# Kernel tuning notes

Hardware: AMD Instinct MI355X
Metric: run time of the kernel (lower is better)

Reference implementation:

```python
import jax, jax.numpy as jnp
import numpy as np

N_NODES = 50000
N_EDGES = 800000
D = 256


def setup_inputs() -> dict:
    key = jax.random.key(0)
    k_x, k_e, k_w1, k_w2 = jax.random.split(key, 4)
    x = jax.random.normal(k_x, (N_NODES, D), dtype=jnp.float32)
    edge_index = jax.random.randint(k_e, (2, N_EDGES), 0, N_NODES, dtype=jnp.int64)
    # attention MLP params (Linear(d, d//2) -> ReLU -> Linear(d//2, 1) -> Sigmoid)
    W1 = jax.random.normal(k_w1, (D, D // 2), dtype=jnp.float32) * (1.0 / np.sqrt(D))
    b1 = jnp.zeros((D // 2,), dtype=jnp.float32)
    W2 = jax.random.normal(k_w2, (D // 2, 1), dtype=jnp.float32) * (1.0 / np.sqrt(D // 2))
    b2 = jnp.zeros((1,), dtype=jnp.float32)
    return {"x": x, "edge_index": edge_index, "W1": W1, "b1": b1, "W2": W2, "b2": b2}


def reference(x, edge_index, W1, b1, W2, b2):
    # mean aggregation with attention: for each destination node i (row),
    # weighted mean of neighbor (col) features with sigmoid-MLP attention weights.
    row, col = edge_index[0], edge_index[1]
    neigh = x[col]                                   # [E, D] gathered neighbor features
    h = jax.nn.relu(neigh @ W1 + b1)                 # [E, D//2]
    w = jax.nn.sigmoid(h @ W2 + b2)                  # [E, 1] attention weight per edge
    num = jax.ops.segment_sum(neigh * w, row, num_segments=N_NODES)  # [N, D]
    den = jax.ops.segment_sum(w, row, num_segments=N_NODES)          # [N, 1]
    # nodes with no neighbors stay zero (matching the torch loop's skip)
    out = jnp.where(den > 0, num / jnp.maximum(den, 1e-12), 0.0)
    return out
```

## Files before the change

kernel.cpp:

```cpp
#include <hip/hip_runtime.h>
#include <hip/hip_bf16.h>

#define D 256
#define DH 128
#define NB 8

typedef __attribute__((ext_vector_type(8))) short short8;
typedef __attribute__((ext_vector_type(4))) float floatx4;
typedef __attribute__((ext_vector_type(4))) unsigned int uintx4;

__device__ __forceinline__ int eload(const void* p, long long i, int is64) {
    if (is64) return (int)((const long long*)p)[i];
    return ((const int*)p)[i];
}

__device__ __forceinline__ unsigned pack_bf16(unsigned a, unsigned b) {
    unsigned ra = (a + 0x7fffu + ((a >> 16) & 1u)) >> 16;
    unsigned rb = (b + 0x7fffu + ((b >> 16) & 1u)) & 0xffff0000u;
    return ra | rb;
}
__device__ __forceinline__ unsigned short bf16_of(float f) {
    unsigned u = __float_as_uint(f);
    return (unsigned short)((u + 0x7fffu + ((u >> 16) & 1u)) >> 16);
}

__global__ __launch_bounds__(256) void prep_kernel(const float* __restrict__ W1,
                                                   uint4* __restrict__ Bp,
                                                   const int* __restrict__ ei,
                                                   int* __restrict__ flag, int E,
                                                   int* __restrict__ cursor,
                                                   int N, int pad) {
    if (blockIdx.x >= 17) {
        int total4 = (N * pad) >> 2;
        uint4* c4 = (uint4*)cursor;
        uint4 z = make_uint4(0u, 0u, 0u, 0u);
        for (int i = (blockIdx.x - 17) * 256 + threadIdx.x; i < total4;
             i += (gridDim.x - 17) * 256)
            c4[i] = z;
        if (blockIdx.x == 17 && threadIdx.x == 0) {
            for (int i = total4 * 4; i < N * pad; ++i) cursor[i] = 0;
        }
        return;
    }
    if (blockIdx.x == 16) {
        int tid = threadIdx.x;
        if (tid == 0) *flag = 0;
        __syncthreads();
        int limit = min(E, 4096);
        int v = 0;
        for (int i = tid; i < limit; i += 256) v |= ei[2 * i + 1];
#pragma unroll
        for (int off = 32; off > 0; off >>= 1) v |= __shfl_down(v, off, 64);
        if ((tid & 63) == 0) atomicOr(flag, v);
        return;
    }
    int t = blockIdx.x * 256 + threadIdx.x;
    int lane = t & 63;
    int kt = (t >> 6) & 7;
    int nt = t >> 9;
    int col = nt * 16 + (lane & 15);
    int k0 = kt * 32 + (lane >> 4) * 8;
    unsigned v[8];
#pragma unroll
    for (int j = 0; j < 8; ++j) v[j] = __float_as_uint(W1[(k0 + j) * DH + col]);
    uint4 o;
    o.x = pack_bf16(v[0], v[1]);
    o.y = pack_bf16(v[2], v[3]);
    o.z = pack_bf16(v[4], v[5]);
    o.w = pack_bf16(v[6], v[7]);
    Bp[t] = o;
}

__global__ __launch_bounds__(256) void score_scatter_kernel(
        const float* __restrict__ x, const uint4* __restrict__ Bp,
        const float* __restrict__ b1, const float* __restrict__ W2,
        const float* __restrict__ b2, uint2* __restrict__ xb,
        float* __restrict__ s,
        const void* __restrict__ ep, const int* __restrict__ flag,
        int* __restrict__ cursor, unsigned short* __restrict__ cols,
        int cap, int pad, int N, int E, int SB) {
    if ((int)blockIdx.x >= SB) {
        int is64 = (*flag == 0);
        int base = (blockIdx.x - SB) * 2048 + threadIdx.x;
        int r[8], c[8];
        bool vld[8];
#pragma unroll
        for (int j = 0; j < 8; ++j) {
            int e = base + j * 256;
            vld[j] = (e < E);
            if (vld[j]) {
                r[j] = eload(ep, e, is64);
                c[j] = eload(ep, (long long)E + e, is64);
            }
        }
#pragma unroll
        for (int j = 0; j < 8; ++j) {
            if (vld[j]) {
                int p = atomicAdd(&cursor[r[j] * pad], 1);
                if (p < cap)
                    __builtin_nontemporal_store((unsigned short)c[j],
                                                &cols[(size_t)r[j] * cap + p]);
            }
        }
        return;
    }

    __shared__ __align__(16) uint2 lds[64 * 64];
    int tid = threadIdx.x;
    int blk = blockIdx.x;
    long long n64 = (long long)N * 64;

    long long gbase = (long long)blk * 4096 + tid;
#pragma unroll
    for (int i = 0; i < 16; ++i) {
        long long g = gbase + i * 256;
        int idx = i * 256 + tid;
        if (g < n64) {
            uint4 f = ((const uint4*)x)[g];
            uint2 o;
            o.x = pack_bf16(f.x, f.y);
            o.y = pack_bf16(f.z, f.w);
            xb[g] = o;
            int row = idx >> 6, cc = idx & 63;
            lds[row * 64 + (cc ^ ((row & 7) << 1))] = o;
        }
    }
    __syncthreads();

    int lane = tid & 63;
    int wid = tid >> 6;
    int quad = lane >> 4;
    int rbase = blk * 64 + wid * 16;
    int lrow = wid * 16 + (lane & 15);
    int fx = (lrow & 7) << 1;

    short8 afrag[8];
#pragma unroll
    for (int kt = 0; kt < 8; ++kt) {
        int e = kt * 8 + quad * 2;
        afrag[kt] = *(const short8*)&lds[lrow * 64 + (e ^ fx)];
    }

    const short8* Bs = (const short8*)Bp;
    float z0 = 0.f, z1 = 0.f, z2 = 0.f, z3 = 0.f;
#pragma unroll
    for (int nt = 0; nt < 8; ++nt) {
        floatx4 acc = {0.f, 0.f, 0.f, 0.f};
#pragma unroll
        for (int kt = 0; kt < 8; ++kt) {
            short8 b = Bs[(nt * 8 + kt) * 64 + lane];
            acc = __builtin_amdgcn_mfma_f32_16x16x32_bf16(afrag[kt], b, acc, 0, 0, 0);
        }
        int col = nt * 16 + (lane & 15);
        float b1c = b1[col], w2c = W2[col];
        z0 += fmaxf(acc[0] + b1c, 0.f) * w2c;
        z1 += fmaxf(acc[1] + b1c, 0.f) * w2c;
        z2 += fmaxf(acc[2] + b1c, 0.f) * w2c;
        z3 += fmaxf(acc[3] + b1c, 0.f) * w2c;
    }

#pragma unroll
    for (int off = 1; off < 16; off <<= 1) {
        z0 += __shfl_xor(z0, off, 64);
        z1 += __shfl_xor(z1, off, 64);
        z2 += __shfl_xor(z2, off, 64);
        z3 += __shfl_xor(z3, off, 64);
    }
    if ((lane & 15) == 0) {
        float b2v = b2[0];
        int r = rbase + quad * 4;
        float zz[4] = {z0, z1, z2, z3};
#pragma unroll
        for (int j = 0; j < 4; ++j)
            if (r + j < N) s[r + j] = 1.f / (1.f + __expf(-(zz[j] + b2v)));
    }
}

__device__ __forceinline__ float4 unpack_bf16x4(uint2 v) {
    float4 r;
    r.x = __uint_as_float(v.x << 16);
    r.y = __uint_as_float(v.x & 0xffff0000u);
    r.z = __uint_as_float(v.y << 16);
    r.w = __uint_as_float(v.y & 0xffff0000u);
    return r;
}

__global__ __launch_bounds__(256) void agg_u16_kernel(const uint2* __restrict__ xb,
                                                      const float* __restrict__ s,
                                                      const int* __restrict__ cursor,
                                                      const unsigned short* __restrict__ cols,
                                                      int cap, int pad,
                                                      float4* __restrict__ out4, int N) {
    int lane = threadIdx.x & 63;
    int node = blockIdx.x * 4 + (threadIdx.x >> 6);
    if (node >= N) return;
    int cnt = min(cursor[node * pad], cap);
    const unsigned short* mc = cols + (size_t)node * cap;

    float4 acc = make_float4(0.f, 0.f, 0.f, 0.f);
    float den = 0.f;
    int k = 0;
    for (; k + 8 <= cnt; k += 8) {
        uintx4 cc = __builtin_nontemporal_load((const uintx4*)(mc + k));
        int c0 = cc.x & 0xffff, c1 = cc.x >> 16;
        int c2 = cc.y & 0xffff, c3 = cc.y >> 16;
        int c4 = cc.z & 0xffff, c5 = cc.z >> 16;
        int c6 = cc.w & 0xffff, c7 = cc.w >> 16;
        float s0 = s[c0], s1 = s[c1], s2 = s[c2], s3 = s[c3];
        float s4 = s[c4], s5 = s[c5], s6 = s[c6], s7 = s[c7];
        uint2 v0 = xb[(size_t)c0 * 64 + lane];
        uint2 v1 = xb[(size_t)c1 * 64 + lane];
        uint2 v2 = xb[(size_t)c2 * 64 + lane];
        uint2 v3 = xb[(size_t)c3 * 64 + lane];
        uint2 v4 = xb[(size_t)c4 * 64 + lane];
        uint2 v5 = xb[(size_t)c5 * 64 + lane];
        uint2 v6 = xb[(size_t)c6 * 64 + lane];
        uint2 v7 = xb[(size_t)c7 * 64 + lane];
        float4 f0 = unpack_bf16x4(v0);
        float4 f1 = unpack_bf16x4(v1);
        float4 f2 = unpack_bf16x4(v2);
        float4 f3 = unpack_bf16x4(v3);
        float4 f4 = unpack_bf16x4(v4);
        float4 f5 = unpack_bf16x4(v5);
        float4 f6 = unpack_bf16x4(v6);
        float4 f7 = unpack_bf16x4(v7);
        acc.x = fmaf(f0.x, s0, fmaf(f1.x, s1, fmaf(f2.x, s2, fmaf(f3.x, s3, acc.x))));
        acc.y = fmaf(f0.y, s0, fmaf(f1.y, s1, fmaf(f2.y, s2, fmaf(f3.y, s3, acc.y))));
        acc.z = fmaf(f0.z, s0, fmaf(f1.z, s1, fmaf(f2.z, s2, fmaf(f3.z, s3, acc.z))));
        acc.w = fmaf(f0.w, s0, fmaf(f1.w, s1, fmaf(f2.w, s2, fmaf(f3.w, s3, acc.w))));
        acc.x = fmaf(f4.x, s4, fmaf(f5.x, s5, fmaf(f6.x, s6, fmaf(f7.x, s7, acc.x))));
        acc.y = fmaf(f4.y, s4, fmaf(f5.y, s5, fmaf(f6.y, s6, fmaf(f7.y, s7, acc.y))));
        acc.z = fmaf(f4.z, s4, fmaf(f5.z, s5, fmaf(f6.z, s6, fmaf(f7.z, s7, acc.z))));
        acc.w = fmaf(f4.w, s4, fmaf(f5.w, s5, fmaf(f6.w, s6, fmaf(f7.w, s7, acc.w))));
        den += ((s0 + s1) + (s2 + s3)) + ((s4 + s5) + (s6 + s7));
    }
    for (; k + 4 <= cnt; k += 4) {
        uint2 cc = *(const uint2*)(mc + k);
        int c0 = cc.x & 0xffff, c1 = cc.x >> 16;
        int c2 = cc.y & 0xffff, c3 = cc.y >> 16;
        float s0 = s[c0], s1 = s[c1], s2 = s[c2], s3 = s[c3];
        uint2 v0 = xb[(size_t)c0 * 64 + lane];
        uint2 v1 = xb[(size_t)c1 * 64 + lane];
        uint2 v2 = xb[(size_t)c2 * 64 + lane];
        uint2 v3 = xb[(size_t)c3 * 64 + lane];
        float4 f0 = unpack_bf16x4(v0);
        float4 f1 = unpack_bf16x4(v1);
        float4 f2 = unpack_bf16x4(v2);
        float4 f3 = unpack_bf16x4(v3);
        acc.x = fmaf(f0.x, s0, fmaf(f1.x, s1, fmaf(f2.x, s2, fmaf(f3.x, s3, acc.x))));
        acc.y = fmaf(f0.y, s0, fmaf(f1.y, s1, fmaf(f2.y, s2, fmaf(f3.y, s3, acc.y))));
        acc.z = fmaf(f0.z, s0, fmaf(f1.z, s1, fmaf(f2.z, s2, fmaf(f3.z, s3, acc.z))));
        acc.w = fmaf(f0.w, s0, fmaf(f1.w, s1, fmaf(f2.w, s2, fmaf(f3.w, s3, acc.w))));
        den += (s0 + s1) + (s2 + s3);
    }
    for (; k < cnt; ++k) {
        int c0 = mc[k];
        float s0 = s[c0];
        float4 f0 = unpack_bf16x4(xb[(size_t)c0 * 64 + lane]);
        acc.x = fmaf(f0.x, s0, acc.x);
        acc.y = fmaf(f0.y, s0, acc.y);
        acc.z = fmaf(f0.z, s0, acc.z);
        acc.w = fmaf(f0.w, s0, acc.w);
        den += s0;
    }
    floatx4 o = {0.f, 0.f, 0.f, 0.f};
    if (cnt > 0) {
        float inv = 1.f / den;
        o.x = acc.x * inv; o.y = acc.y * inv; o.z = acc.z * inv; o.w = acc.w * inv;
    }
    __builtin_nontemporal_store(o, (floatx4*)&out4[(size_t)node * 64 + lane]);
}

__global__ __launch_bounds__(256) void detect_kernel(const int* __restrict__ ei,
                                                     int* __restrict__ flag, int E) {
    int tid = threadIdx.x;
    int limit = min(E, 4096);
    int v = 0;
    for (int i = tid; i < limit; i += 256) v |= ei[2 * i + 1];
#pragma unroll
    for (int off = 32; off > 0; off >>= 1) v |= __shfl_down(v, off, 64);
    if ((tid & 63) == 0) atomicOr(flag, v);
}

__global__ __launch_bounds__(256) void score_kernel(const float* __restrict__ x,
                                                    const float* __restrict__ W1,
                                                    const float* __restrict__ b1,
                                                    const float* __restrict__ W2,
                                                    const float* __restrict__ b2,
                                                    float* __restrict__ s, int N) {
    __shared__ __align__(16) float xs[4][NB][D];
    int lane = threadIdx.x & 63;
    int wid  = threadIdx.x >> 6;
    int base = (blockIdx.x * 4 + wid) * NB;
#pragma unroll
    for (int m = 0; m < NB; ++m) {
        int n = base + m;
        float4 v = make_float4(0.f, 0.f, 0.f, 0.f);
        if (n < N) v = ((const float4*)x)[(size_t)n * 64 + lane];
        ((float4*)&xs[wid][m][0])[lane] = v;
    }
    __syncthreads();
    float h0[NB], h1[NB];
#pragma unroll
    for (int m = 0; m < NB; ++m) { h0[m] = 0.f; h1[m] = 0.f; }
#pragma unroll 4
    for (int k = 0; k < D; ++k) {
        float w1a = W1[k * DH + lane];
        float w1b = W1[k * DH + 64 + lane];
#pragma unroll
        for (int m = 0; m < NB; ++m) {
            float xv = xs[wid][m][k];
            h0[m] = fmaf(xv, w1a, h0[m]);
            h1[m] = fmaf(xv, w1b, h1[m]);
        }
    }
    float b1a = b1[lane], b1b = b1[lane + 64];
    float w2a = W2[lane], w2b = W2[lane + 64];
    float b2v = b2[0];
#pragma unroll
    for (int m = 0; m < NB; ++m) {
        float za = fmaxf(h0[m] + b1a, 0.f) * w2a + fmaxf(h1[m] + b1b, 0.f) * w2b;
#pragma unroll
        for (int off = 32; off > 0; off >>= 1) za += __shfl_down(za, off, 64);
        if (lane == 0) {
            int n = base + m;
            if (n < N) s[n] = 1.f / (1.f + __expf(-(za + b2v)));
        }
    }
}

__global__ __launch_bounds__(256) void hist_kernel(const void* __restrict__ ep,
                                                   const int* __restrict__ flag,
                                                   int* __restrict__ cnt, int E) {
    int is64 = (*flag == 0);
    int e = blockIdx.x * blockDim.x + threadIdx.x;
    if (e < E) atomicAdd(&cnt[eload(ep, e, is64)], 1);
}

__global__ __launch_bounds__(256) void bucket_kernel(const int* __restrict__ cnt,
                                                     int* __restrict__ beg,
                                                     int* __restrict__ cursor,
                                                     int* __restrict__ total, int N) {
    int i = blockIdx.x * blockDim.x + threadIdx.x;
    int lane = threadIdx.x & 63;
    int v = (i < N) ? cnt[i] : 0;
    int inc = v;
#pragma unroll
    for (int off = 1; off < 64; off <<= 1) {
        int t = __shfl_up(inc, off, 64);
        if (lane >= off) inc += t;
    }
    int base = 0;
    if (lane == 63) base = atomicAdd(total, inc);
    base = __shfl(base, 63, 64);
    if (i < N) {
        int b = base + inc - v;
        beg[i] = b;
        cursor[i] = b;
    }
}

__global__ __launch_bounds__(256) void scatter32_kernel(const void* __restrict__ ep,
                                                        const int* __restrict__ flag,
                                                        int* __restrict__ cursor,
                                                        int* __restrict__ cols, int E) {
    int is64 = (*flag == 0);
    int e = blockIdx.x * blockDim.x + threadIdx.x;
    if (e < E) {
        int r = eload(ep, e, is64);
        int c = eload(ep, (long long)E + e, is64);
        int p = atomicAdd(&cursor[r], 1);
        cols[p] = c;
    }
}

__global__ __launch_bounds__(256) void agg_f32_kernel(const float4* __restrict__ x4,
                                                      const float* __restrict__ s,
                                                      const int* __restrict__ begs,
                                                      const int* __restrict__ cnt,
                                                      const int* __restrict__ cols,
                                                      float4* __restrict__ out4, int N) {
    int lane = threadIdx.x & 63;
    int node = blockIdx.x * 4 + (threadIdx.x >> 6);
    if (node >= N) return;
    int beg = begs[node], end = beg + cnt[node];
    float4 acc = make_float4(0.f, 0.f, 0.f, 0.f);
    float den = 0.f;
    for (int k = beg; k < end; ++k) {
        int c = cols[k];
        float sc = s[c];
        float4 xv = x4[(size_t)c * 64 + lane];
        acc.x = fmaf(xv.x, sc, acc.x);
        acc.y = fmaf(xv.y, sc, acc.y);
        acc.z = fmaf(xv.z, sc, acc.z);
        acc.w = fmaf(xv.w, sc, acc.w);
        den += sc;
    }
    float4 o = make_float4(0.f, 0.f, 0.f, 0.f);
    if (end > beg) {
        float inv = 1.f / den;
        o.x = acc.x * inv; o.y = acc.y * inv; o.z = acc.z * inv; o.w = acc.w * inv;
    }
    out4[(size_t)node * 64 + lane] = o;
}

extern "C" void kernel_launch(void* const* d_in, const int* in_sizes, int n_in,
                              void* d_out, int out_size, void* d_ws, size_t ws_size,
                              hipStream_t stream) {
    const float* x  = (const float*)d_in[0];
    const void*  ei = d_in[1];
    const float* W1 = (const float*)d_in[2];
    const float* b1 = (const float*)d_in[3];
    const float* W2 = (const float*)d_in[4];
    const float* b2 = (const float*)d_in[5];
    int N = in_sizes[0] / D;
    int E = in_sizes[1] / 2;

    char* ws = (char*)d_ws;

    auto plan = [&](int cap, int pad, size_t& oCur, size_t& oS, size_t& oCols,
                    size_t& oBp, size_t& oXb) -> size_t {
        oCur  = 16;
        oS    = (oCur + (size_t)N * pad * 4 + 15) & ~15ull;
        oCols = (oS + (size_t)N * 4 + 255) & ~255ull;
        oBp   = (oCols + (size_t)N * cap * 2 + 255) & ~255ull;
        oXb   = (oBp + 65536 + 255) & ~255ull;
        return oXb + (size_t)N * D * 2;
    };

    int cap = 96, pad = 16;
    size_t oCur, oS, oCols, oBp, oXb;
    size_t need = plan(cap, pad, oCur, oS, oCols, oBp, oXb);
    if (need > ws_size) { pad = 4;  need = plan(cap, pad, oCur, oS, oCols, oBp, oXb); }
    if (need > ws_size) { pad = 1;  need = plan(cap, pad, oCur, oS, oCols, oBp, oXb); }
    if (need > ws_size) { cap = 64; need = plan(cap, pad, oCur, oS, oCols, oBp, oXb); }

    if (N <= 65536 && need <= ws_size) {
        int*            flag   = (int*)(ws);
        int*            cursor = (int*)(ws + oCur);
        float*          s      = (float*)(ws + oS);
        unsigned short* cols   = (unsigned short*)(ws + oCols);
        uint4*          Bpack  = (uint4*)(ws + oBp);
        uint2*          xb     = (uint2*)(ws + oXb);

        const int ZB = 256;
        prep_kernel<<<17 + ZB, 256, 0, stream>>>(W1, Bpack, (const int*)ei, flag, E,
                                                 cursor, N, pad);

        int SB = (N + 63) / 64;
        int TBe = (E + 2047) / 2048;
        score_scatter_kernel<<<SB + TBe, 256, 0, stream>>>(x, Bpack, b1, W2, b2,
                                                           xb, s, ei, flag, cursor,
                                                           cols, cap, pad, N, E, SB);
        agg_u16_kernel<<<(N + 3) / 4, 256, 0, stream>>>(xb, s, cursor, cols, cap, pad,
                                                        (float4*)d_out, N);
        return;
    }

    size_t o0 = 0;
    size_t o1 = 16;
    size_t o2 = (o1 + (size_t)N * 4 + 15) & ~15ull;
    size_t o3 = (o2 + (size_t)N * 4 + 15) & ~15ull;
    size_t o4 = (o3 + (size_t)N * 4 + 15) & ~15ull;
    size_t o5 = (o4 + (size_t)N * 4 + 15) & ~15ull;
    int*   flag   = (int*)(ws + o0);
    int*   total  = (int*)(ws + o0 + 4);
    int*   cnt    = (int*)(ws + o1);
    int*   beg    = (int*)(ws + o2);
    int*   cursor = (int*)(ws + o3);
    float* s      = (float*)(ws + o4);
    int*   cols   = (int*)(ws + o5);

    hipMemsetAsync(ws, 0, o1 + (size_t)N * 4, stream);
    detect_kernel<<<1, 256, 0, stream>>>((const int*)ei, flag, E);
    score_kernel<<<(N + 4 * NB - 1) / (4 * NB), 256, 0, stream>>>(x, W1, b1, W2, b2, s, N);
    hist_kernel<<<(E + 255) / 256, 256, 0, stream>>>(ei, flag, cnt, E);
    bucket_kernel<<<(N + 255) / 256, 256, 0, stream>>>(cnt, beg, cursor, total, N);
    scatter32_kernel<<<(E + 255) / 256, 256, 0, stream>>>(ei, flag, cursor, cols, E);
    agg_f32_kernel<<<(N + 3) / 4, 256, 0, stream>>>((const float4*)x, s, beg, cnt, cols,
                                                    (float4*)d_out, N);
}
```

Baseline: 205.6 us.

## Slice-major bf16 feature layout with sentinel-filled adjacency and sliced aggregation

Stores the bf16 copy of x in eight 32-feature slices, each node-major, and splits aggregation so every block handles one slice. Within a wave, the eight lanes of each octet cover one neighbor, so eight neighbors are processed in parallel and then reduced with shuffles. The adjacency buffer is pre-filled with a 0xffff sentinel, so aggregation no longer reads the per-node counter. The score kernel reads its MFMA A-fragments back from global xb instead of LDS, and the per-node capacity drops from 96 to 64. This aims to improve gather locality and latency hiding, at the cost of reading the column lists eight times, an extra fill pass, and a limit of 65535 nodes.

New measurement: 298.7 us. 45.3% more time.

```diff
diff --git a/kernel.cpp b/kernel.cpp
--- a/kernel.cpp
+++ b/kernel.cpp
@@ -19,9 +19,14 @@
     unsigned rb = (b + 0x7fffu + ((b >> 16) & 1u)) & 0xffff0000u;
     return ra | rb;
 }
-__device__ __forceinline__ unsigned short bf16_of(float f) {
-    unsigned u = __float_as_uint(f);
-    return (unsigned short)((u + 0x7fffu + ((u >> 16) & 1u)) >> 16);
+
+__device__ __forceinline__ float4 unpack_bf16x4(uint2 v) {
+    float4 r;
+    r.x = __uint_as_float(v.x << 16);
+    r.y = __uint_as_float(v.x & 0xffff0000u);
+    r.z = __uint_as_float(v.y << 16);
+    r.w = __uint_as_float(v.y & 0xffff0000u);
+    return r;
 }
 
 __global__ __launch_bounds__(256) void prep_kernel(const float* __restrict__ W1,
@@ -29,16 +34,22 @@
                                                    const int* __restrict__ ei,
                                                    int* __restrict__ flag, int E,
                                                    int* __restrict__ cursor,
-                                                   int N, int pad) {
+                                                   unsigned short* __restrict__ cols,
+                                                   int cap, int N, int pad) {
     if (blockIdx.x >= 17) {
+        int stride = (gridDim.x - 17) * 256;
+        int tid0 = (blockIdx.x - 17) * 256 + threadIdx.x;
         int total4 = (N * pad) >> 2;
         uint4* c4 = (uint4*)cursor;
         uint4 z = make_uint4(0u, 0u, 0u, 0u);
-        for (int i = (blockIdx.x - 17) * 256 + threadIdx.x; i < total4;
-             i += (gridDim.x - 17) * 256)
-            c4[i] = z;
+        for (int i = tid0; i < total4; i += stride) c4[i] = z;
+        int colQ = (N * cap) >> 3;
+        uint4* q4 = (uint4*)cols;
+        uint4 f = make_uint4(~0u, ~0u, ~0u, ~0u);
+        for (int i = tid0; i < colQ; i += stride) q4[i] = f;
         if (blockIdx.x == 17 && threadIdx.x == 0) {
             for (int i = total4 * 4; i < N * pad; ++i) cursor[i] = 0;
+            for (int i = colQ * 8; i < N * cap; ++i) cols[i] = 0xffffu;
         }
         return;
     }
@@ -78,7 +89,7 @@
         float* __restrict__ s,
         const void* __restrict__ ep, const int* __restrict__ flag,
         int* __restrict__ cursor, unsigned short* __restrict__ cols,
-        int cap, int pad, int N, int E, int SB) {
+        int cap, int pad, int Npad, int N, int E, int SB) {
     if ((int)blockIdx.x >= SB) {
         int is64 = (*flag == 0);
         int base = (blockIdx.x - SB) * 2048 + threadIdx.x;
@@ -105,10 +116,10 @@
         return;
     }
 
-    __shared__ __align__(16) uint2 lds[64 * 64];
     int tid = threadIdx.x;
     int blk = blockIdx.x;
     long long n64 = (long long)N * 64;
+    int npad8 = Npad * 8;
 
     long long gbase = (long long)blk * 4096 + tid;
 #pragma unroll
@@ -116,13 +127,13 @@
         long long g = gbase + i * 256;
         int idx = i * 256 + tid;
         if (g < n64) {
-            uint4 f = ((const uint4*)x)[g];
+            uint4 fv = ((const uint4*)x)[g];
             uint2 o;
-            o.x = pack_bf16(f.x, f.y);
-            o.y = pack_bf16(f.z, f.w);
-            xb[g] = o;
+            o.x = pack_bf16(fv.x, fv.y);
+            o.y = pack_bf16(fv.z, fv.w);
             int row = idx >> 6, cc = idx & 63;
-            lds[row * 64 + (cc ^ ((row & 7) << 1))] = o;
+            int nodeid = blk * 64 + row;
+            xb[(size_t)(cc >> 3) * npad8 + (size_t)nodeid * 8 + (cc & 7)] = o;
         }
     }
     __syncthreads();
@@ -131,15 +142,12 @@
     int wid = tid >> 6;
     int quad = lane >> 4;
     int rbase = blk * 64 + wid * 16;
-    int lrow = wid * 16 + (lane & 15);
-    int fx = (lrow & 7) << 1;
+    int lnode = rbase + (lane & 15);
 
     short8 afrag[8];
 #pragma unroll
-    for (int kt = 0; kt < 8; ++kt) {
-        int e = kt * 8 + quad * 2;
-        afrag[kt] = *(const short8*)&lds[lrow * 64 + (e ^ fx)];
-    }
+    for (int kt = 0; kt < 8; ++kt)
+        afrag[kt] = *(const short8*)&xb[(size_t)kt * npad8 + (size_t)lnode * 8 + quad * 2];
 
     const short8* Bs = (const short8*)Bp;
     float z0 = 0.f, z1 = 0.f, z2 = 0.f, z3 = 0.f;
@@ -176,99 +184,65 @@
     }
 }
 
-__device__ __forceinline__ float4 unpack_bf16x4(uint2 v) {
-    float4 r;
-    r.x = __uint_as_float(v.x << 16);
-    r.y = __uint_as_float(v.x & 0xffff0000u);
-    r.z = __uint_as_float(v.y << 16);
-    r.w = __uint_as_float(v.y & 0xffff0000u);
-    return r;
-}
-
-__global__ __launch_bounds__(256) void agg_u16_kernel(const uint2* __restrict__ xb,
-                                                      const float* __restrict__ s,
-                                                      const int* __restrict__ cursor,
-                                                      const unsigned short* __restrict__ cols,
-                                                      int cap, int pad,
-                                                      float4* __restrict__ out4, int N) {
+__global__ __launch_bounds__(256) void agg_slice_kernel(
+        const uint2* __restrict__ xb, const float* __restrict__ s,
+        const unsigned short* __restrict__ cols,
+        int cap, int Npad, float4* __restrict__ out4, int N) {
+    int slice = blockIdx.x & 7;
+    int group = blockIdx.x >> 3;
+    int wid = threadIdx.x >> 6;
     int lane = threadIdx.x & 63;
-    int node = blockIdx.x * 4 + (threadIdx.x >> 6);
+    int oct = lane >> 3;
+    int dl  = lane & 7;
+    int node = group * 4 + wid;
     if (node >= N) return;
-    int cnt = min(cursor[node * pad], cap);
-    const unsigned short* mc = cols + (size_t)node * cap;
+
+    const uint4* mc4 = (const uint4*)(cols + (size_t)node * cap);
+    const uint2* xbs = xb + (size_t)slice * Npad * 8;
 
     float4 acc = make_float4(0.f, 0.f, 0.f, 0.f);
     float den = 0.f;
-    int k = 0;
-    for (; k + 8 <= cnt; k += 8) {
-        uintx4 cc = __builtin_nontemporal_load((const uintx4*)(mc + k));
-        int c0 = cc.x & 0xffff, c1 = cc.x >> 16;
-        int c2 = cc.y & 0xffff, c3 = cc.y >> 16;
-        int c4 = cc.z & 0xffff, c5 = cc.z >> 16;
-        int c6 = cc.w & 0xffff, c7 = cc.w >> 16;
-        float s0 = s[c0], s1 = s[c1], s2 = s[c2], s3 = s[c3];
-        float s4 = s[c4], s5 = s[c5], s6 = s[c6], s7 = s[c7];
-        uint2 v0 = xb[(size_t)c0 * 64 + lane];
-        uint2 v1 = xb[(size_t)c1 * 64 + lane];
-        uint2 v2 = xb[(size_t)c2 * 64 + lane];
-        uint2 v3 = xb[(size_t)c3 * 64 + lane];
-        uint2 v4 = xb[(size_t)c4 * 64 + lane];
-        uint2 v5 = xb[(size_t)c5 * 64 + lane];
-        uint2 v6 = xb[(size_t)c6 * 64 + lane];
-        uint2 v7 = xb[(size_t)c7 * 64 + lane];
-        float4 f0 = unpack_bf16x4(v0);
-        float4 f1 = unpack_bf16x4(v1);
-        float4 f2 = unpack_bf16x4(v2);
-        float4 f3 = unpack_bf16x4(v3);
-        float4 f4 = unpack_bf16x4(v4);
-        float4 f5 = unpack_bf16x4(v5);
-        float4 f6 = unpack_bf16x4(v6);
-        float4 f7 = unpack_bf16x4(v7);
-        acc.x = fmaf(f0.x, s0, fmaf(f1.x, s1, fmaf(f2.x, s2, fmaf(f3.x, s3, acc.x))));
-        acc.y = fmaf(f0.y, s0, fmaf(f1.y, s1, fmaf(f2.y, s2, fmaf(f3.y, s3, acc.y))));
-        acc.z = fmaf(f0.z, s0, fmaf(f1.z, s1, fmaf(f2.z, s2, fmaf(f3.z, s3, acc.z))));
-        acc.w = fmaf(f0.w, s0, fmaf(f1.w, s1, fmaf(f2.w, s2, fmaf(f3.w, s3, acc.w))));
-        acc.x = fmaf(f4.x, s4, fmaf(f5.x, s5, fmaf(f6.x, s6, fmaf(f7.x, s7, acc.x))));
-        acc.y = fmaf(f4.y, s4, fmaf(f5.y, s5, fmaf(f6.y, s6, fmaf(f7.y, s7, acc.y))));
-        acc.z = fmaf(f4.z, s4, fmaf(f5.z, s5, fmaf(f6.z, s6, fmaf(f7.z, s7, acc.z))));
-        acc.w = fmaf(f4.w, s4, fmaf(f5.w, s5, fmaf(f6.w, s6, fmaf(f7.w, s7, acc.w))));
-        den += ((s0 + s1) + (s2 + s3)) + ((s4 + s5) + (s6 + s7));
-    }
-    for (; k + 4 <= cnt; k += 4) {
-        uint2 cc = *(const uint2*)(mc + k);
-        int c0 = cc.x & 0xffff, c1 = cc.x >> 16;
-        int c2 = cc.y & 0xffff, c3 = cc.y >> 16;
-        float s0 = s[c0], s1 = s[c1], s2 = s[c2], s3 = s[c3];
-        uint2 v0 = xb[(size_t)c0 * 64 + lane];
-        uint2 v1 = xb[(size_t)c1 * 64 + lane];
-        uint2 v2 = xb[(size_t)c2 * 64 + lane];
-        uint2 v3 = xb[(size_t)c3 * 64 + lane];
-        float4 f0 = unpack_bf16x4(v0);
-        float4 f1 = unpack_bf16x4(v1);
-        float4 f2 = unpack_bf16x4(v2);
-        float4 f3 = unpack_bf16x4(v3);
-        acc.x = fmaf(f0.x, s0, fmaf(f1.x, s1, fmaf(f2.x, s2, fmaf(f3.x, s3, acc.x))));
-        acc.y = fmaf(f0.y, s0, fmaf(f1.y, s1, fmaf(f2.y, s2, fmaf(f3.y, s3, acc.y))));
-        acc.z = fmaf(f0.z, s0, fmaf(f1.z, s1, fmaf(f2.z, s2, fmaf(f3.z, s3, acc.z))));
-        acc.w = fmaf(f0.w, s0, fmaf(f1.w, s1, fmaf(f2.w, s2, fmaf(f3.w, s3, acc.w))));
-        den += (s0 + s1) + (s2 + s3);
-    }
-    for (; k < cnt; ++k) {
-        int c0 = mc[k];
-        float s0 = s[c0];
-        float4 f0 = unpack_bf16x4(xb[(size_t)c0 * 64 + lane]);
-        acc.x = fmaf(f0.x, s0, acc.x);
-        acc.y = fmaf(f0.y, s0, acc.y);
-        acc.z = fmaf(f0.z, s0, acc.z);
-        acc.w = fmaf(f0.w, s0, acc.w);
-        den += s0;
-    }
-    floatx4 o = {0.f, 0.f, 0.f, 0.f};
-    if (cnt > 0) {
-        float inv = 1.f / den;
-        o.x = acc.x * inv; o.y = acc.y * inv; o.z = acc.z * inv; o.w = acc.w * inv;
-    }
-    __builtin_nontemporal_store(o, (floatx4*)&out4[(size_t)node * 64 + lane]);
+    int chunks = cap >> 3;
+    uint4 cv = mc4[0];
+    for (int i = 0; i < chunks; ++i) {
+        if ((cv.x & 0xffffu) == 0xffffu) break;
+        uint4 cn;
+        if (i + 1 < chunks) cn = mc4[i + 1];
+        else cn = make_uint4(~0u, ~0u, ~0u, ~0u);
+        unsigned cw = (oct & 4) ? ((oct & 2) ? cv.w : cv.z)
+                                : ((oct & 2) ? cv.y : cv.x);
+        unsigned col = (oct & 1) ? (cw >> 16) : (cw & 0xffffu);
+        bool valid = (col != 0xffffu);
+        int ci = valid ? (int)col : 0;
+        float sv = s[ci];
+        sv = valid ? sv : 0.f;
+        uint2 v = xbs[(size_t)ci * 8 + dl];
+        float4 f = unpack_bf16x4(v);
+        acc.x = fmaf(f.x, sv, acc.x);
+        acc.y = fmaf(f.y, sv, acc.y);
+        acc.z = fmaf(f.z, sv, acc.z);
+        acc.w = fmaf(f.w, sv, acc.w);
+        den += sv;
+        cv = cn;
+    }
+#pragma unroll
+    for (int off = 8; off < 64; off <<= 1) {
+        acc.x += __shfl_xor(acc.x, off, 64);
+        acc.y += __shfl_xor(acc.y, off, 64);
+        acc.z += __shfl_xor(acc.z, off, 64);
+        acc.w += __shfl_xor(acc.w, off, 64);
+        den   += __shfl_xor(den,   off, 64);
+    }
+    if (oct == 0) {
+        floatx4 o = {0.f, 0.f, 0.f, 0.f};
+        if (den > 0.f) {
+            float inv = 1.f / den;
+            o.x = acc.x * inv; o.y = acc.y * inv;
+            o.z = acc.z * inv; o.w = acc.w * inv;
+        }
+        __builtin_nontemporal_store(
+            o, (floatx4*)&out4[(size_t)node * 64 + slice * 8 + dl]);
+    }
 }
 
 __global__ __launch_bounds__(256) void detect_kernel(const int* __restrict__ ei,
@@ -417,6 +391,7 @@
     int E = in_sizes[1] / 2;
 
     char* ws = (char*)d_ws;
+    int Npad = (N + 63) & ~63;
 
     auto plan = [&](int cap, int pad, size_t& oCur, size_t& oS, size_t& oCols,
                     size_t& oBp, size_t& oXb) -> size_t {
@@ -425,17 +400,16 @@
         oCols = (oS + (size_t)N * 4 + 255) & ~255ull;
         oBp   = (oCols + (size_t)N * cap * 2 + 255) & ~255ull;
         oXb   = (oBp + 65536 + 255) & ~255ull;
-        return oXb + (size_t)N * D * 2;
+        return oXb + (size_t)Npad * D * 2;
     };
 
-    int cap = 96, pad = 16;
+    int cap = 64, pad = 16;
     size_t oCur, oS, oCols, oBp, oXb;
     size_t need = plan(cap, pad, oCur, oS, oCols, oBp, oXb);
     if (need > ws_size) { pad = 4;  need = plan(cap, pad, oCur, oS, oCols, oBp, oXb); }
     if (need > ws_size) { pad = 1;  need = plan(cap, pad, oCur, oS, oCols, oBp, oXb); }
-    if (need > ws_size) { cap = 64; need = plan(cap, pad, oCur, oS, oCols, oBp, oXb); }
-
-    if (N <= 65536 && need <= ws_size) {
+
+    if (N <= 65535 && need <= ws_size) {
         int*            flag   = (int*)(ws);
         int*            cursor = (int*)(ws + oCur);
         float*          s      = (float*)(ws + oS);
@@ -445,15 +419,17 @@
 
         const int ZB = 256;
         prep_kernel<<<17 + ZB, 256, 0, stream>>>(W1, Bpack, (const int*)ei, flag, E,
-                                                 cursor, N, pad);
+                                                 cursor, cols, cap, N, pad);
 
         int SB = (N + 63) / 64;
         int TBe = (E + 2047) / 2048;
         score_scatter_kernel<<<SB + TBe, 256, 0, stream>>>(x, Bpack, b1, W2, b2,
                                                            xb, s, ei, flag, cursor,
-                                                           cols, cap, pad, N, E, SB);
-        agg_u16_kernel<<<(N + 3) / 4, 256, 0, stream>>>(xb, s, cursor, cols, cap, pad,
-                                                        (float4*)d_out, N);
+                                                           cols, cap, pad, Npad,
+                                                           N, E, SB);
+        int G4 = (N + 3) / 4;
+        agg_slice_kernel<<<G4 * 8, 256, 0, stream>>>(xb, s, cols, cap, Npad,
+                                                     (float4*)d_out, N);
         return;
     }
 
```
